# Kernel optimization log

Measured on AMD Instinct MI355X. Metric: run time of the kernel, lower is better.

Reference implementation:

```python
import math
import jax
import jax.numpy as jnp
import numpy as np

N_IMG = 8
A = 3
H = 100
W = 100
STRIDE = 16
IMG = 1600
PRE_NMS_TOP_N = 2000
POST_NMS_TOP_N = 1000
NMS_THRESH = 0.7
MIN_SIZE = 0
BBOX_XFORM_CLIP = math.log(1000.0 / 16.0)


def setup_inputs() -> dict:
    key = jax.random.key(0)
    k1, k2 = jax.random.split(key)
    objectness = jax.random.normal(k1, (N_IMG, A, H, W), jnp.float32)
    box_regression = jax.random.normal(k2, (N_IMG, A * 4, H, W), jnp.float32) * 0.5
    # Grid anchors, flattened in (H, W, A) order to match objectness.permute(0,2,3,1)
    cy = (jnp.arange(H, dtype=jnp.float32) + 0.5) * STRIDE  # [H]
    cx = (jnp.arange(W, dtype=jnp.float32) + 0.5) * STRIDE  # [W]
    half = jnp.array([64.0, 128.0, 256.0], jnp.float32) / 2.0  # [A]
    cy = cy[:, None, None]  # [H,1,1]
    cx = cx[None, :, None]  # [1,W,1]
    s = half[None, None, :]  # [1,1,A]
    x1, y1, x2, y2 = jnp.broadcast_arrays(cx - s, cy - s, cx + s, cy + s)
    anc = jnp.stack([x1, y1, x2, y2], axis=-1).reshape(-1, 4)  # [H*W*A, 4]
    anchors = jnp.broadcast_to(anc[None], (N_IMG, H * W * A, 4)).copy()
    return {
        "objectness": objectness,
        "box_regression": box_regression,
        "anchors": anchors,
        "image_height": IMG,
        "image_width": IMG,
    }


def _decode(deltas, boxes):
    # BoxCoder(weights=(1,1,1,1)).decode with TO_REMOVE=1
    widths = boxes[..., 2] - boxes[..., 0] + 1.0
    heights = boxes[..., 3] - boxes[..., 1] + 1.0
    ctr_x = boxes[..., 0] + 0.5 * widths
    ctr_y = boxes[..., 1] + 0.5 * heights
    dx, dy = deltas[..., 0], deltas[..., 1]
    dw = jnp.minimum(deltas[..., 2], BBOX_XFORM_CLIP)
    dh = jnp.minimum(deltas[..., 3], BBOX_XFORM_CLIP)
    pcx = dx * widths + ctr_x
    pcy = dy * heights + ctr_y
    pw = jnp.exp(dw) * widths
    ph = jnp.exp(dh) * heights
    return jnp.stack(
        [pcx - 0.5 * pw, pcy - 0.5 * ph, pcx + 0.5 * pw - 1.0, pcy + 0.5 * ph - 1.0],
        axis=-1,
    )


def _nms_keep(boxes, valid, thresh):
    # boxes [n,4] sorted by descending score; valid: pre-filter mask.
    n = boxes.shape[0]
    x1, y1, x2, y2 = boxes[:, 0], boxes[:, 1], boxes[:, 2], boxes[:, 3]
    areas = (x2 - x1 + 1.0) * (y2 - y1 + 1.0)
    xx1 = jnp.maximum(x1[:, None], x1[None, :])
    yy1 = jnp.maximum(y1[:, None], y1[None, :])
    xx2 = jnp.minimum(x2[:, None], x2[None, :])
    yy2 = jnp.minimum(y2[:, None], y2[None, :])
    inter = jnp.maximum(xx2 - xx1 + 1.0, 0.0) * jnp.maximum(yy2 - yy1 + 1.0, 0.0)
    iou = inter / (areas[:, None] + areas[None, :] - inter)
    idx = jnp.arange(n)

    def body(i, keep):
        sup = keep[i] & (iou[i] > thresh) & (idx > i)
        return keep & ~sup

    return jax.lax.fori_loop(0, n, body, valid)


def _forward(objectness, box_regression, anchors, image_height, image_width):
    N, A_, H_, W_ = objectness.shape
    scores = jax.nn.sigmoid(objectness.transpose(0, 2, 3, 1).reshape(N, -1))  # [N, A*H*W]
    deltas = (
        box_regression.reshape(N, A_, 4, H_, W_)
        .transpose(0, 3, 4, 1, 2)
        .reshape(N, -1, 4)
    )
    pre = min(PRE_NMS_TOP_N, scores.shape[1])
    top_scores, top_idx = jax.lax.top_k(scores, pre)  # sorted descending
    deltas = jnp.take_along_axis(deltas, top_idx[:, :, None], axis=1)
    anc = jnp.take_along_axis(anchors, top_idx[:, :, None], axis=1)
    props = _decode(deltas, anc)  # [N, pre, 4]
    # clip to image (fact = 1)
    xs = jnp.clip(props[..., 0::2], 0.0, image_width - 1.0)
    ys = jnp.clip(props[..., 1::2], 0.0, image_height - 1.0)
    props = jnp.stack([xs[..., 0], ys[..., 0], xs[..., 1], ys[..., 1]], axis=-1)
    # filter small / out-of-image-center boxes
    ws = props[..., 2] - props[..., 0] + 1.0
    hs = props[..., 3] - props[..., 1] + 1.0
    xc = props[..., 0] + ws / 2.0
    yc = props[..., 1] + hs / 2.0
    valid = (ws >= MIN_SIZE) & (hs >= MIN_SIZE) & (xc < image_width) & (yc < image_height)
    keep = jax.vmap(lambda b, v: _nms_keep(b, v, NMS_THRESH))(props, valid)

    def _select(b, s, k):
        # compact kept boxes (already score-sorted) into fixed-size output
        rank = jnp.cumsum(k) - 1
        tgt = jnp.where(k & (rank < POST_NMS_TOP_N), rank, POST_NMS_TOP_N)
        ob = jnp.zeros((POST_NMS_TOP_N + 1, 4), b.dtype).at[tgt].set(b)[:POST_NMS_TOP_N]
        os = jnp.zeros((POST_NMS_TOP_N + 1,), s.dtype).at[tgt].set(s)[:POST_NMS_TOP_N]
        ov = jnp.arange(POST_NMS_TOP_N) < jnp.minimum(jnp.sum(k), POST_NMS_TOP_N)
        return ob, os, ov

    return jax.vmap(_select)(props, top_scores, keep)


def reference(objectness, box_regression, anchors, image_height, image_width):
    # Returns (boxes [N,post,4], objectness scores [N,post], valid mask [N,post])
    return _forward(objectness, box_regression, anchors, image_height, image_width)
```

## Files before the change

kernel.cpp:

```cpp
#include <hip/hip_runtime.h>
#include <math.h>
#include <stdint.h>

#define NIMG   8
#define NA     30000
#define NQ4    7500
#define PRE_N  2000
#define POST_N 1000
#define NMS_TH 0.7f
#define DCLIP  4.135166556742356f
#define IMGF   1600.0f
#define IMGM1  1599.0f
#define CAND_MAX 4096
#define HPITCH 4104
#define BIG_BIN 64
#define PREF_BIN 3064u


__device__ __forceinline__ void decode_store(
    uint64_t key, unsigned int rank, int n, const float* __restrict__ breg,
    float* __restrict__ wsBoxes, float* __restrict__ wsScores,
    int* __restrict__ wsValid)
{
    unsigned int idx = (unsigned int)key;
    unsigned int k   = ~((unsigned int)(key >> 32));
    unsigned int u   = (k & 0x80000000u) ? (k & 0x7fffffffu) : ~k;
    float logit = __uint_as_float(u);
    float score = 1.0f / (1.0f + expf(-logit));

    int a = idx % 3, t = idx / 3, w = t % 100, h = t / 100;
    const float* bp = breg + n*120000 + (a*4)*10000 + t;
    float dx = bp[0], dy = bp[10000], dw = bp[20000], dh = bp[30000];

    float half = (a == 0) ? 32.0f : ((a == 1) ? 64.0f : 128.0f);
    float cx = w * 16.0f + 8.0f, cy = h * 16.0f + 8.0f;
    float x1 = cx - half, y1 = cy - half, x2 = cx + half, y2 = cy + half;
    float wd = x2 - x1 + 1.0f, hg = y2 - y1 + 1.0f;
    float cxr = x1 + 0.5f * wd, cyr = y1 + 0.5f * hg;
    dw = fminf(dw, DCLIP); dh = fminf(dh, DCLIP);
    float pcx = dx * wd + cxr, pcy = dy * hg + cyr;
    float pw = expf(dw) * wd, ph = expf(dh) * hg;
    float px1 = pcx - 0.5f * pw, py1 = pcy - 0.5f * ph;
    float px2 = pcx + 0.5f * pw - 1.0f, py2 = pcy + 0.5f * ph - 1.0f;
    px1 = fminf(fmaxf(px1, 0.0f), IMGM1);
    px2 = fminf(fmaxf(px2, 0.0f), IMGM1);
    py1 = fminf(fmaxf(py1, 0.0f), IMGM1);
    py2 = fminf(fmaxf(py2, 0.0f), IMGM1);
    float wss = px2 - px1 + 1.0f, hss = py2 - py1 + 1.0f;
    float xc = px1 + wss * 0.5f, yc = py1 + hss * 0.5f;
    int valid = (wss >= 0.0f) && (hss >= 0.0f) && (xc < IMGF) && (yc < IMGF);

    ((float4*)wsBoxes)[n * PRE_N + (int)rank] = make_float4(px1, py1, px2, py2);
    wsScores[n * PRE_N + (int)rank] = score;
    wsValid [n * PRE_N + (int)rank] = valid;
}

__device__ __forceinline__ unsigned int keyof(float f) {
    unsigned int u = __float_as_uint(f);
    return (u & 0x80000000u) ? ~u : (u | 0x80000000u);
}

__global__ __launch_bounds__(1024) void topk_decode(
    const float* __restrict__ obj, const float* __restrict__ breg,
    float* __restrict__ wsBoxes, float* __restrict__ wsScores,
    int* __restrict__ wsValid)
{
    const int n    = blockIdx.x;
    const int tid  = threadIdx.x;
    const int lane = tid & 63;
    const int wid  = tid >> 6;
    const int rep  = wid & 3;

    __shared__ unsigned int   histf[4 * HPITCH];
    __shared__ unsigned short sufx[4096];
    __shared__ uint64_t       grp[CAND_MAX];
    __shared__ uint64_t       grp2[CAND_MAX];
    __shared__ unsigned int   wsum[16];
    __shared__ unsigned int   sbstar;
    __shared__ unsigned int   lbbase[16];
    __shared__ unsigned int   lbcnt, lbtot;

    unsigned int*   hist2  = histf;
    unsigned short* sufx2  = (unsigned short*)(histf + HPITCH);
    unsigned char*  bin2lb = (unsigned char*)(histf + 2 * HPITCH);

    for (int b = tid; b < 4 * HPITCH; b += 1024) histf[b] = 0u;
    __syncthreads();

    const float4* obj4 = (const float4*)(obj + n * NA);
    float4 v[8];
    #pragma unroll
    for (int kk = 0; kk < 7; ++kk) v[kk] = obj4[tid + kk * 1024];
    v[7] = make_float4(0.f, 0.f, 0.f, 0.f);
    if (tid < NQ4 - 7 * 1024) v[7] = obj4[tid + 7 * 1024];

    #pragma unroll
    for (int kk = 0; kk < 8; ++kk) {
        if (kk == 7 && tid >= NQ4 - 7 * 1024) continue;
        const float fv[4] = {v[kk].x, v[kk].y, v[kk].z, v[kk].w};
        #pragma unroll
        for (int e = 0; e < 4; ++e) {
            unsigned int b = keyof(fv[e]) >> 20;
            if (b >= PREF_BIN)
                atomicAdd(&histf[rep * HPITCH + b], 1u);
        }
    }
    __syncthreads();

    unsigned int c0, c1, c2, c3;
    {
        const int b0 = tid * 4;
        c0 = histf[b0+0] + histf[HPITCH+b0+0] + histf[2*HPITCH+b0+0] + histf[3*HPITCH+b0+0];
        c1 = histf[b0+1] + histf[HPITCH+b0+1] + histf[2*HPITCH+b0+1] + histf[3*HPITCH+b0+1];
        c2 = histf[b0+2] + histf[HPITCH+b0+2] + histf[2*HPITCH+b0+2] + histf[3*HPITCH+b0+2];
        c3 = histf[b0+3] + histf[HPITCH+b0+3] + histf[2*HPITCH+b0+3] + histf[3*HPITCH+b0+3];
    }
    unsigned int p = c0 + c1 + c2 + c3;
    unsigned int s = p;
    #pragma unroll
    for (int off = 1; off < 64; off <<= 1) {
        unsigned int vv = __shfl_down(s, off);
        if (lane + off < 64) s += vv;
    }
    if (lane == 0) wsum[wid] = s;
    __syncthreads();
    unsigned int ftotal = 0;
    for (int w = 0; w < 16; ++w) ftotal += wsum[w];

    if (ftotal < PRE_N) {
        #pragma unroll
        for (int kk = 0; kk < 8; ++kk) {
            if (kk == 7 && tid >= NQ4 - 7 * 1024) continue;
            const float fv[4] = {v[kk].x, v[kk].y, v[kk].z, v[kk].w};
            #pragma unroll
            for (int e = 0; e < 4; ++e) {
                unsigned int b = keyof(fv[e]) >> 20;
                if (b < PREF_BIN)
                    atomicAdd(&histf[rep * HPITCH + b], 1u);
            }
        }
        __syncthreads();
        {
            const int b0 = tid * 4;
            c0 = histf[b0+0] + histf[HPITCH+b0+0] + histf[2*HPITCH+b0+0] + histf[3*HPITCH+b0+0];
            c1 = histf[b0+1] + histf[HPITCH+b0+1] + histf[2*HPITCH+b0+1] + histf[3*HPITCH+b0+1];
            c2 = histf[b0+2] + histf[HPITCH+b0+2] + histf[2*HPITCH+b0+2] + histf[3*HPITCH+b0+2];
            c3 = histf[b0+3] + histf[HPITCH+b0+3] + histf[2*HPITCH+b0+3] + histf[3*HPITCH+b0+3];
        }
        p = c0 + c1 + c2 + c3;
        s = p;
        #pragma unroll
        for (int off = 1; off < 64; off <<= 1) {
            unsigned int vv = __shfl_down(s, off);
            if (lane + off < 64) s += vv;
        }
        __syncthreads();
        if (lane == 0) wsum[wid] = s;
        __syncthreads();
    }

    unsigned int wafter = 0;
    for (int w = wid + 1; w < 16; ++w) wafter += wsum[w];
    unsigned int after = (s - p) + wafter;
    {
        unsigned int S3 = after + c3;
        unsigned int S2 = S3 + c2;
        unsigned int S1 = S2 + c1;
        unsigned int S0 = S1 + c0;
        if (S3 >= PRE_N && after < PRE_N) { sbstar = tid*4+3; }
        if (S2 >= PRE_N && S3    < PRE_N) { sbstar = tid*4+2; }
        if (S1 >= PRE_N && S2    < PRE_N) { sbstar = tid*4+1; }
        if (S0 >= PRE_N && S1    < PRE_N) { sbstar = tid*4+0; }
        sufx[tid*4+0] = (unsigned short)S1;
        sufx[tid*4+1] = (unsigned short)S2;
        sufx[tid*4+2] = (unsigned short)S3;
        sufx[tid*4+3] = (unsigned short)after;

        const unsigned int st[4] = {S1, S2, S3, after};
        #pragma unroll
        for (int q = 0; q < 4; ++q) {
            const int b = tid*4 + q;
            unsigned int base = st[q];
            #pragma unroll
            for (int r = 0; r < 4; ++r) {
                unsigned int c = histf[r * HPITCH + b];
                histf[r * HPITCH + b] = base;
                base += c;
            }
        }
    }
    __syncthreads();
    const unsigned int bstar = sbstar;

    #pragma unroll
    for (int kk = 0; kk < 8; ++kk) {
        if (kk == 7 && tid >= NQ4 - 7 * 1024) continue;
        const float fv[4] = {v[kk].x, v[kk].y, v[kk].z, v[kk].w};
        #pragma unroll
        for (int e = 0; e < 4; ++e) {
            unsigned int k = keyof(fv[e]);
            unsigned int b = k >> 20;
            if (b < bstar) continue;
            int j = (tid + kk * 1024) * 4 + e;
            int a = j / 10000, t = j - a * 10000;
            uint64_t key = (((uint64_t)(~k)) << 32) | (unsigned int)(t * 3 + a);
            unsigned int slot = atomicAdd(&histf[rep * HPITCH + b], 1u);
            if (slot < CAND_MAX) grp[slot] = key;
        }
    }
    __syncthreads();

    const unsigned int total = min(histf[3 * HPITCH + bstar], (unsigned int)CAND_MAX);

    ((unsigned int*)bin2lb)[tid] = 0xFFFFFFFFu;
    hist2[tid] = 0u; hist2[tid+1024] = 0u; hist2[tid+2048] = 0u; hist2[tid+3072] = 0u;
    if (tid == 0) { lbcnt = 0u; lbtot = 0u; }
    __syncthreads();

    #pragma unroll
    for (int q = 0; q < 4; ++q) {
        const unsigned int b = (unsigned int)(tid*4 + q);
        if (b >= bstar) {
            const unsigned int ge  = min(histf[3*HPITCH + b], (unsigned int)CAND_MAX);
            const unsigned int cnt = ge - (unsigned int)sufx[b];
            if (cnt > (unsigned int)BIG_BIN) {
                unsigned int pos = atomicAdd(&lbcnt, 1u);
                if (pos < 16u) {
                    bin2lb[b] = (unsigned char)pos;
                    lbbase[pos] = atomicAdd(&lbtot, cnt);
                }
            }
        }
    }
    __syncthreads();

    for (unsigned int slot = tid; slot < total; slot += 1024) {
        const unsigned int hi = (unsigned int)(grp[slot] >> 32);
        const unsigned int b  = 4095u - (hi >> 20);
        const unsigned char lb = bin2lb[b];
        if (lb != 0xFFu)
            atomicAdd(&hist2[(unsigned int)lb * 256u + ((hi >> 12) & 0xFFu)], 1u);
    }
    __syncthreads();

    {
        const unsigned int nlb = min(lbcnt, 16u);
        if ((unsigned int)wid < nlb) {
            const int xb = wid * 256 + lane * 4;
            unsigned int e0 = hist2[xb+0], e1 = hist2[xb+1],
                         e2 = hist2[xb+2], e3 = hist2[xb+3];
            unsigned int tsum = e0 + e1 + e2 + e3;
            unsigned int inc = tsum;
            #pragma unroll
            for (int off = 1; off < 64; off <<= 1) {
                unsigned int vv = __shfl_up(inc, off);
                if (lane >= off) inc += vv;
            }
            unsigned int base = lbbase[wid] + (inc - tsum);
            hist2[xb+0] = base;             sufx2[xb+0] = (unsigned short)base;
            base += e0; hist2[xb+1] = base; sufx2[xb+1] = (unsigned short)base;
            base += e1; hist2[xb+2] = base; sufx2[xb+2] = (unsigned short)base;
            base += e2; hist2[xb+3] = base; sufx2[xb+3] = (unsigned short)base;
        }
    }
    __syncthreads();

    for (unsigned int slot = tid; slot < total; slot += 1024) {
        const uint64_t key = grp[slot];
        const unsigned int hi = (unsigned int)(key >> 32);
        const unsigned int b  = 4095u - (hi >> 20);
        const unsigned char lb = bin2lb[b];
        if (lb != 0xFFu) {
            unsigned int d = atomicAdd(&hist2[(unsigned int)lb * 256u + ((hi >> 12) & 0xFFu)], 1u);
            grp2[d] = key;
        }
    }
    __syncthreads();

    for (unsigned int slot = tid; slot < total; slot += 1024) {
        const uint64_t key = grp[slot];
        const unsigned int hi = (unsigned int)(key >> 32);
        const unsigned int b  = 4095u - (hi >> 20);
        const unsigned int gbeg = sufx[b];
        const unsigned int gend = min(histf[3 * HPITCH + b], (unsigned int)CAND_MAX);
        const unsigned char lb  = bin2lb[b];
        unsigned int rank;

        if (lb != 0xFFu) {
            const unsigned int x   = (unsigned int)lb * 256u + ((hi >> 12) & 0xFFu);
            const unsigned int s2  = sufx2[x];
            const unsigned int e2v = hist2[x];
            rank = gbeg + (s2 - lbbase[lb]);
            for (unsigned int g = s2; g < e2v; g += 8u) {
                #pragma unroll
                for (int i = 0; i < 8; ++i) {
                    const unsigned int gi = g + (unsigned int)i;
                    const uint64_t vv = grp2[min(gi, e2v - 1u)];
                    rank += (gi < e2v && vv < key) ? 1u : 0u;
                }
            }
        } else {
            rank = gbeg;
            unsigned int g = gbeg;
            for (; g + 8u <= gend; g += 8u) {
                uint64_t v0 = grp[g+0], v1 = grp[g+1], v2 = grp[g+2], v3 = grp[g+3];
                uint64_t v4 = grp[g+4], v5 = grp[g+5], v6 = grp[g+6], v7 = grp[g+7];
                unsigned int r0 = (v0 < key) ? 1u : 0u;
                r0 += (v1 < key) ? 1u : 0u;
                r0 += (v2 < key) ? 1u : 0u;
                r0 += (v3 < key) ? 1u : 0u;
                r0 += (v4 < key) ? 1u : 0u;
                r0 += (v5 < key) ? 1u : 0u;
                r0 += (v6 < key) ? 1u : 0u;
                r0 += (v7 < key) ? 1u : 0u;
                rank += r0;
            }
            for (; g < gend; ++g)
                rank += (grp[g] < key) ? 1u : 0u;
        }
        if (rank >= PRE_N) continue;
        decode_store(key, rank, n, breg, wsBoxes, wsScores, wsValid);
    }
}

__global__ __launch_bounds__(512) void nms_mask(
    const float* __restrict__ wsBoxes, uint64_t* __restrict__ mask)
{
    const int blk  = blockIdx.x;
    const int n    = blk >> 5;
    const int i_t  = blk & 31;
    const int tid  = threadIdx.x;
    const int lane = tid & 63;
    const int wv   = tid >> 6;

    __shared__ uint64_t tile[64 * 33];

    for (int idx = tid; idx < 64 * 33; idx += 512) tile[idx] = 0ull;
    __syncthreads();

    const int r = i_t * 64 + lane;
    float4 rb = (r < PRE_N) ? ((const float4*)wsBoxes)[n * PRE_N + r]
                            : make_float4(0.f, 0.f, 0.f, 0.f);
    float ra = (rb.z - rb.x + 1.0f) * (rb.w - rb.y + 1.0f);

    for (int j_t = i_t + wv; j_t < 32; j_t += 8) {
        const int j = j_t * 64 + lane;
        float4 cb = (j < PRE_N) ? ((const float4*)wsBoxes)[n * PRE_N + j]
                                : make_float4(3e30f, 3e30f, 3e30f, 3e30f);
        float ca = (cb.z - cb.x + 1.0f) * (cb.w - cb.y + 1.0f);
        const uint64_t jmask = (j_t == 31) ? 0xFFFFull : ~0ull;
        const bool diag = (j_t == i_t);
        uint64_t myword = 0ull;

        #pragma unroll
        for (int c = 0; c < 64; ++c) {
            float rx1 = __int_as_float(__builtin_amdgcn_readlane(__float_as_int(rb.x), c));
            float ry1 = __int_as_float(__builtin_amdgcn_readlane(__float_as_int(rb.y), c));
            float rx2 = __int_as_float(__builtin_amdgcn_readlane(__float_as_int(rb.z), c));
            float ry2 = __int_as_float(__builtin_amdgcn_readlane(__float_as_int(rb.w), c));
            float rar = __int_as_float(__builtin_amdgcn_readlane(__float_as_int(ra), c));
            float xx1 = fmaxf(rx1, cb.x), yy1 = fmaxf(ry1, cb.y);
            float xx2 = fminf(rx2, cb.z), yy2 = fminf(ry2, cb.w);
            float ww = fmaxf(xx2 - xx1 + 1.0f, 0.0f);
            float hh = fmaxf(yy2 - yy1 + 1.0f, 0.0f);
            float inter = ww * hh;
            float denom = rar + ca - inter;
            unsigned long long bits = __ballot(inter > NMS_TH * denom) & jmask;
            if (diag) bits &= (c == 63) ? 0ull : ((~0ull) << (c + 1));
            if (lane == c) myword = bits;
        }
        tile[lane * 33 + j_t] = myword;
    }
    __syncthreads();

    uint64_t* mrow = mask + ((size_t)n * PRE_N + (size_t)i_t * 64) * 32;
    const int cmax = (i_t == 31) ? 16 : 64;
    for (int idx = tid; idx < cmax * 32; idx += 512) {
        const int rr = idx >> 5, w = idx & 31;
        mrow[idx] = tile[rr * 33 + w];
    }
}

#define SL(n,b) \
    "global_load_dword v" #n ", %[voff], %[sbase]\n\t" \
    "v_add_u32 %[voff], 0x100, %[voff]\n\t"

#define SS(n,b) \
    "s_waitcnt vmcnt(63)\n\t" \
    "v_readlane_b32 %[t], v" #n ", %[lw]\n\t" \
    "s_bitcmp1_b32 %[win], " #b "\n\t" \
    "s_cselect_b32 %[m], 0, -1\n\t" \
    "s_sub_i32 %[kept], %[kept], %[m]\n\t" \
    "s_and_b32 %[t], %[t], %[m]\n\t" \
    "s_or_b32 %[win], %[win], %[t]\n\t" \
    "v_and_b32 v" #n ", %[m], v" #n "\n\t" \
    "v_or_b32 %[rem], %[rem], v" #n "\n\t" \
    "global_load_dword v" #n ", %[voff], %[sbase]\n\t" \
    "v_add_u32 %[voff], 0x100, %[voff]\n\t"

#define SN(n,b,w) \
    "s_waitcnt vmcnt(" #w ")\n\t" \
    "v_readlane_b32 %[t], v" #n ", %[lw]\n\t" \
    "s_bitcmp1_b32 %[win], " #b "\n\t" \
    "s_cselect_b32 %[m], 0, -1\n\t" \
    "s_sub_i32 %[kept], %[kept], %[m]\n\t" \
    "s_and_b32 %[t], %[t], %[m]\n\t" \
    "s_or_b32 %[win], %[win], %[t]\n\t" \
    "v_and_b32 v" #n ", %[m], v" #n "\n\t" \
    "v_or_b32 %[rem], %[rem], v" #n "\n\t"

#define SWIN \
    "s_add_u32 %[lw], %[lw], 1\n\t" \
    "v_readlane_b32 %[t], %[rem], %[lw]\n\t" \
    "s_mov_b32 %[win], %[t]\n\t"

#define ROW_A(M) M(64,0) M(65,1) M(66,2) M(67,3) M(68,4) M(69,5) M(70,6) M(71,7) \
    M(72,8) M(73,9) M(74,10) M(75,11) M(76,12) M(77,13) M(78,14) M(79,15) \
    M(80,16) M(81,17) M(82,18) M(83,19) M(84,20) M(85,21) M(86,22) M(87,23) \
    M(88,24) M(89,25) M(90,26) M(91,27) M(92,28) M(93,29) M(94,30) M(95,31)
#define ROW_B(M) M(96,0) M(97,1) M(98,2) M(99,3) M(100,4) M(101,5) M(102,6) M(103,7) \
    M(104,8) M(105,9) M(106,10) M(107,11) M(108,12) M(109,13) M(110,14) M(111,15) \
    M(112,16) M(113,17) M(114,18) M(115,19) M(116,20) M(117,21) M(118,22) M(119,23) \
    M(120,24) M(121,25) M(122,26) M(123,27) M(124,28) M(125,29) M(126,30) M(127,31)

__global__ __launch_bounds__(256) void nms_scan_select(
    const float* __restrict__ wsBoxes, const float* __restrict__ wsScores,
    const int* __restrict__ wsValid, const uint64_t* __restrict__ mask,
    float* __restrict__ out)
{
    const int n   = blockIdx.x;
    const int tid = threadIdx.x;

    __shared__ __align__(8) unsigned char invb[256];
    __shared__ unsigned int keepw32[64];
    __shared__ int sscan[256];

    unsigned int byte = 0xFFu;
    if (tid < PRE_N / 8) {
        byte = 0u;
        for (int q = 0; q < 8; ++q)
            byte |= (wsValid[n * PRE_N + tid * 8 + q] ? 0u : 1u) << q;
    }
    invb[tid] = (unsigned char)byte;
    __syncthreads();

    if (tid < 64) {
        unsigned int rem = ((const unsigned int*)invb)[tid];
        unsigned long long sbase =
            (unsigned long long)(const void*)(mask + (size_t)n * PRE_N * 32);
        unsigned int voff = (unsigned int)(tid * 4);
        int win_, m_, t_, lw_, kept_, cnt_;

        asm volatile(
            "s_waitcnt vmcnt(0) lgkmcnt(0)\n\t"
            "s_mov_b32 %[kept], 0\n\t"
            "s_mov_b32 %[lw], 0\n\t"
            ROW_A(SL) ROW_B(SL)
            "v_readlane_b32 %[t], %[rem], %[lw]\n\t"
            "s_mov_b32 %[win], %[t]\n\t"
            "s_mov_b32 %[cnt], 30\n\t"
            "Lnms_%=:\n\t"
            ROW_A(SS)
            SWIN
            ROW_B(SS)
            SWIN
            "s_cmp_ge_i32 %[kept], 0x3e8\n\t"
            "s_cbranch_scc1 Lend_%=\n\t"
            "s_sub_u32 %[cnt], %[cnt], 1\n\t"
            "s_cmp_lg_u32 %[cnt], 0\n\t"
            "s_cbranch_scc1 Lnms_%=\n\t"
            SS(64,0) SS(65,1) SS(66,2) SS(67,3) SS(68,4) SS(69,5) SS(70,6) SS(71,7)
            SS(72,8) SS(73,9) SS(74,10) SS(75,11) SS(76,12) SS(77,13) SS(78,14) SS(79,15)
            SN(80,16,63) SN(81,17,62) SN(82,18,61) SN(83,19,60)
            SN(84,20,59) SN(85,21,58) SN(86,22,57) SN(87,23,56)
            SN(88,24,55) SN(89,25,54) SN(90,26,53) SN(91,27,52)
            SN(92,28,51) SN(93,29,50) SN(94,30,49) SN(95,31,48)
            SWIN
            SN(96,0,47) SN(97,1,46) SN(98,2,45) SN(99,3,44)
            SN(100,4,43) SN(101,5,42) SN(102,6,41) SN(103,7,40)
            SN(104,8,39) SN(105,9,38) SN(106,10,37) SN(107,11,36)
            SN(108,12,35) SN(109,13,34) SN(110,14,33) SN(111,15,32)
            SN(112,16,31) SN(113,17,30) SN(114,18,29) SN(115,19,28)
            SN(116,20,27) SN(117,21,26) SN(118,22,25) SN(119,23,24)
            SN(120,24,23) SN(121,25,22) SN(122,26,21) SN(123,27,20)
            SN(124,28,19) SN(125,29,18) SN(126,30,17) SN(127,31,16)
            SWIN
            SN(64,0,15) SN(65,1,14) SN(66,2,13) SN(67,3,12)
            SN(68,4,11) SN(69,5,10) SN(70,6,9) SN(71,7,8)
            SN(72,8,7) SN(73,9,6) SN(74,10,5) SN(75,11,4)
            SN(76,12,3) SN(77,13,2) SN(78,14,1) SN(79,15,0)
            "Lend_%=:\n\t"
            "s_waitcnt vmcnt(0)\n\t"
            : [rem]"+v"(rem), [voff]"+v"(voff),
              [win]"=&s"(win_), [m]"=&s"(m_), [t]"=&s"(t_),
              [lw]"=&s"(lw_), [kept]"=&s"(kept_), [cnt]"=&s"(cnt_)
            : [sbase]"s"(sbase)
            : "scc", "vcc", "memory",
              "v64","v65","v66","v67","v68","v69","v70","v71",
              "v72","v73","v74","v75","v76","v77","v78","v79",
              "v80","v81","v82","v83","v84","v85","v86","v87",
              "v88","v89","v90","v91","v92","v93","v94","v95",
              "v96","v97","v98","v99","v100","v101","v102","v103",
              "v104","v105","v106","v107","v108","v109","v110","v111",
              "v112","v113","v114","v115","v116","v117","v118","v119",
              "v120","v121","v122","v123","v124","v125","v126","v127");

        keepw32[tid] = ~rem;
    }
    __syncthreads();

    int c[8]; const int base8 = tid * 8;
    int lsum = 0;
    for (int q = 0; q < 8; ++q) {
        const int i = base8 + q;
        c[q] = (i < PRE_N) ? (int)((keepw32[i >> 5] >> (i & 31)) & 1u) : 0;
        lsum += c[q];
    }
    sscan[tid] = lsum;
    __syncthreads();
    for (int off = 1; off < 256; off <<= 1) {
        int v = (tid >= off) ? sscan[tid - off] : 0;
        __syncthreads();
        sscan[tid] += v;
        __syncthreads();
    }
    const int excl  = sscan[tid] - lsum;
    const int total = sscan[255];

    float* ob  = out + n * POST_N * 4;
    float* osc = out + NIMG * POST_N * 4 + n * POST_N;
    float* ovd = out + NIMG * POST_N * 5 + n * POST_N;

    for (int i = tid; i < POST_N * 4; i += 256) ob[i] = 0.0f;
    for (int i = tid; i < POST_N; i += 256) osc[i] = 0.0f;
    const int lim = min(total, POST_N);
    for (int i = tid; i < POST_N; i += 256) ovd[i] = (i < lim) ? 1.0f : 0.0f;
    __syncthreads();

    int run = excl;
    for (int q = 0; q < 8; ++q) {
        const int i = base8 + q;
        if (i < PRE_N && c[q]) {
            if (run < POST_N) {
                float4 b = ((const float4*)wsBoxes)[n * PRE_N + i];
                ob[run * 4 + 0] = b.x;
                ob[run * 4 + 1] = b.y;
                ob[run * 4 + 2] = b.z;
                ob[run * 4 + 3] = b.w;
                osc[run] = wsScores[n * PRE_N + i];
            }
            run++;
        }
    }
}

extern "C" void kernel_launch(void* const* d_in, const int* in_sizes, int n_in,
                              void* d_out, int out_size, void* d_ws, size_t ws_size,
                              hipStream_t stream) {
    const float* obj  = (const float*)d_in[0];
    const float* breg = (const float*)d_in[1];
    float* ws        = (float*)d_ws;
    float* wsBoxes   = ws;
    float* wsScores  = ws + 64000;
    int*   wsValid   = (int*)(ws + 80000);
    uint64_t* wsMask = (uint64_t*)(ws + 96000);

    topk_decode<<<NIMG, 1024, 0, stream>>>(obj, breg, wsBoxes, wsScores, wsValid);
    nms_mask<<<NIMG * 32, 512, 0, stream>>>(wsBoxes, wsMask);
    nms_scan_select<<<NIMG, 256, 0, stream>>>(wsBoxes, wsScores, wsValid, wsMask,
                                              (float*)d_out);
}
```

Measured before the change: 153.0 us.

## Replace serial asm NMS scan with block-parallel 64-box group propagation

Replaces the single-wave hand-written assembly scan, which streamed every mask word through one wavefront, with a scheme built on 64-box groups. For each group, wave 0 resolves suppression inside the group from the diagonal mask words using readlane. All 512 threads then OR the kept rows' mask words into a shared suppression bitmap for the later groups using atomics. This targets the serial memory-latency chain of the old scan and reads only the rows of kept boxes. In exchange it adds two block barriers per group and shared-memory atomic contention.

```diff
diff --git a/kernel.cpp b/kernel.cpp
--- a/kernel.cpp
+++ b/kernel.cpp
@@ -381,175 +381,148 @@
     }
 }
 
-#define SL(n,b) \
-    "global_load_dword v" #n ", %[voff], %[sbase]\n\t" \
-    "v_add_u32 %[voff], 0x100, %[voff]\n\t"
-
-#define SS(n,b) \
-    "s_waitcnt vmcnt(63)\n\t" \
-    "v_readlane_b32 %[t], v" #n ", %[lw]\n\t" \
-    "s_bitcmp1_b32 %[win], " #b "\n\t" \
-    "s_cselect_b32 %[m], 0, -1\n\t" \
-    "s_sub_i32 %[kept], %[kept], %[m]\n\t" \
-    "s_and_b32 %[t], %[t], %[m]\n\t" \
-    "s_or_b32 %[win], %[win], %[t]\n\t" \
-    "v_and_b32 v" #n ", %[m], v" #n "\n\t" \
-    "v_or_b32 %[rem], %[rem], v" #n "\n\t" \
-    "global_load_dword v" #n ", %[voff], %[sbase]\n\t" \
-    "v_add_u32 %[voff], 0x100, %[voff]\n\t"
-
-#define SN(n,b,w) \
-    "s_waitcnt vmcnt(" #w ")\n\t" \
-    "v_readlane_b32 %[t], v" #n ", %[lw]\n\t" \
-    "s_bitcmp1_b32 %[win], " #b "\n\t" \
-    "s_cselect_b32 %[m], 0, -1\n\t" \
-    "s_sub_i32 %[kept], %[kept], %[m]\n\t" \
-    "s_and_b32 %[t], %[t], %[m]\n\t" \
-    "s_or_b32 %[win], %[win], %[t]\n\t" \
-    "v_and_b32 v" #n ", %[m], v" #n "\n\t" \
-    "v_or_b32 %[rem], %[rem], v" #n "\n\t"
-
-#define SWIN \
-    "s_add_u32 %[lw], %[lw], 1\n\t" \
-    "v_readlane_b32 %[t], %[rem], %[lw]\n\t" \
-    "s_mov_b32 %[win], %[t]\n\t"
-
-#define ROW_A(M) M(64,0) M(65,1) M(66,2) M(67,3) M(68,4) M(69,5) M(70,6) M(71,7) \
-    M(72,8) M(73,9) M(74,10) M(75,11) M(76,12) M(77,13) M(78,14) M(79,15) \
-    M(80,16) M(81,17) M(82,18) M(83,19) M(84,20) M(85,21) M(86,22) M(87,23) \
-    M(88,24) M(89,25) M(90,26) M(91,27) M(92,28) M(93,29) M(94,30) M(95,31)
-#define ROW_B(M) M(96,0) M(97,1) M(98,2) M(99,3) M(100,4) M(101,5) M(102,6) M(103,7) \
-    M(104,8) M(105,9) M(106,10) M(107,11) M(108,12) M(109,13) M(110,14) M(111,15) \
-    M(112,16) M(113,17) M(114,18) M(115,19) M(116,20) M(117,21) M(118,22) M(119,23) \
-    M(120,24) M(121,25) M(122,26) M(123,27) M(124,28) M(125,29) M(126,30) M(127,31)
-
-__global__ __launch_bounds__(256) void nms_scan_select(
+__global__ __launch_bounds__(512) void nms_scan_select(
     const float* __restrict__ wsBoxes, const float* __restrict__ wsScores,
     const int* __restrict__ wsValid, const uint64_t* __restrict__ mask,
     float* __restrict__ out)
 {
-    const int n   = blockIdx.x;
-    const int tid = threadIdx.x;
-
-    __shared__ __align__(8) unsigned char invb[256];
-    __shared__ unsigned int keepw32[64];
+    const int n    = blockIdx.x;
+    const int tid  = threadIdx.x;
+    const int lane = tid & 63;
+    const int wid  = tid >> 6;
+
+    __shared__ unsigned int sup[64];
+    __shared__ unsigned int kml, kmh;
+    __shared__ int skept, sdone;
     __shared__ int sscan[256];
 
-    unsigned int byte = 0xFFu;
-    if (tid < PRE_N / 8) {
-        byte = 0u;
-        for (int q = 0; q < 8; ++q)
-            byte |= (wsValid[n * PRE_N + tid * 8 + q] ? 0u : 1u) << q;
-    }
-    invb[tid] = (unsigned char)byte;
-    __syncthreads();
-
-    if (tid < 64) {
-        unsigned int rem = ((const unsigned int*)invb)[tid];
-        unsigned long long sbase =
-            (unsigned long long)(const void*)(mask + (size_t)n * PRE_N * 32);
-        unsigned int voff = (unsigned int)(tid * 4);
-        int win_, m_, t_, lw_, kept_, cnt_;
-
-        asm volatile(
-            "s_waitcnt vmcnt(0) lgkmcnt(0)\n\t"
-            "s_mov_b32 %[kept], 0\n\t"
-            "s_mov_b32 %[lw], 0\n\t"
-            ROW_A(SL) ROW_B(SL)
-            "v_readlane_b32 %[t], %[rem], %[lw]\n\t"
-            "s_mov_b32 %[win], %[t]\n\t"
-            "s_mov_b32 %[cnt], 30\n\t"
-            "Lnms_%=:\n\t"
-            ROW_A(SS)
-            SWIN
-            ROW_B(SS)
-            SWIN
-            "s_cmp_ge_i32 %[kept], 0x3e8\n\t"
-            "s_cbranch_scc1 Lend_%=\n\t"
-            "s_sub_u32 %[cnt], %[cnt], 1\n\t"
-            "s_cmp_lg_u32 %[cnt], 0\n\t"
-            "s_cbranch_scc1 Lnms_%=\n\t"
-            SS(64,0) SS(65,1) SS(66,2) SS(67,3) SS(68,4) SS(69,5) SS(70,6) SS(71,7)
-            SS(72,8) SS(73,9) SS(74,10) SS(75,11) SS(76,12) SS(77,13) SS(78,14) SS(79,15)
-            SN(80,16,63) SN(81,17,62) SN(82,18,61) SN(83,19,60)
-            SN(84,20,59) SN(85,21,58) SN(86,22,57) SN(87,23,56)
-            SN(88,24,55) SN(89,25,54) SN(90,26,53) SN(91,27,52)
-            SN(92,28,51) SN(93,29,50) SN(94,30,49) SN(95,31,48)
-            SWIN
-            SN(96,0,47) SN(97,1,46) SN(98,2,45) SN(99,3,44)
-            SN(100,4,43) SN(101,5,42) SN(102,6,41) SN(103,7,40)
-            SN(104,8,39) SN(105,9,38) SN(106,10,37) SN(107,11,36)
-            SN(108,12,35) SN(109,13,34) SN(110,14,33) SN(111,15,32)
-            SN(112,16,31) SN(113,17,30) SN(114,18,29) SN(115,19,28)
-            SN(116,20,27) SN(117,21,26) SN(118,22,25) SN(119,23,24)
-            SN(120,24,23) SN(121,25,22) SN(122,26,21) SN(123,27,20)
-            SN(124,28,19) SN(125,29,18) SN(126,30,17) SN(127,31,16)
-            SWIN
-            SN(64,0,15) SN(65,1,14) SN(66,2,13) SN(67,3,12)
-            SN(68,4,11) SN(69,5,10) SN(70,6,9) SN(71,7,8)
-            SN(72,8,7) SN(73,9,6) SN(74,10,5) SN(75,11,4)
-            SN(76,12,3) SN(77,13,2) SN(78,14,1) SN(79,15,0)
-            "Lend_%=:\n\t"
-            "s_waitcnt vmcnt(0)\n\t"
-            : [rem]"+v"(rem), [voff]"+v"(voff),
-              [win]"=&s"(win_), [m]"=&s"(m_), [t]"=&s"(t_),
-              [lw]"=&s"(lw_), [kept]"=&s"(kept_), [cnt]"=&s"(cnt_)
-            : [sbase]"s"(sbase)
-            : "scc", "vcc", "memory",
-              "v64","v65","v66","v67","v68","v69","v70","v71",
-              "v72","v73","v74","v75","v76","v77","v78","v79",
-              "v80","v81","v82","v83","v84","v85","v86","v87",
-              "v88","v89","v90","v91","v92","v93","v94","v95",
-              "v96","v97","v98","v99","v100","v101","v102","v103",
-              "v104","v105","v106","v107","v108","v109","v110","v111",
-              "v112","v113","v114","v115","v116","v117","v118","v119",
-              "v120","v121","v122","v123","v124","v125","v126","v127");
-
-        keepw32[tid] = ~rem;
-    }
-    __syncthreads();
-
-    int c[8]; const int base8 = tid * 8;
+    if (tid < 64) sup[tid] = 0u;
+    if (tid == 0) { skept = 0; sdone = 0; }
+    __syncthreads();
+
+    if (tid < 500) {
+        int4 vv = ((const int4*)(wsValid + n * PRE_N))[tid];
+        unsigned int nib = (vv.x ? 0u : 1u) | ((vv.y ? 0u : 1u) << 1)
+                         | ((vv.z ? 0u : 1u) << 2) | ((vv.w ? 0u : 1u) << 3);
+        if (nib) atomicOr(&sup[tid >> 3], nib << ((tid & 7) * 4));
+    } else {
+        atomicOr(&sup[tid >> 3], 0xFu << ((tid & 7) * 4));
+    }
+    __syncthreads();
+
+    const uint64_t* mrow = mask + (size_t)n * PRE_N * 32;
+
+    unsigned int cl = 0u, ch = 0u;
+    if (wid == 0) {
+        uint64_t cw = (lane < PRE_N) ? mrow[(size_t)lane * 32 + 0] : 0ull;
+        cl = (unsigned int)cw; ch = (unsigned int)(cw >> 32);
+    }
+
+    for (int g = 0; g < 32; ++g) {
+        __syncthreads();
+        if (sdone) break;
+
+        if (wid == 0) {
+            unsigned int nl = 0u, nh = 0u;
+            if (g < 31) {
+                const int r = (g + 1) * 64 + lane;
+                uint64_t cw = (r < PRE_N) ? mrow[(size_t)r * 32 + (g + 1)] : 0ull;
+                nl = (unsigned int)cw; nh = (unsigned int)(cw >> 32);
+            }
+
+            unsigned long long win =
+                ((unsigned long long)sup[2*g + 1] << 32) | sup[2*g];
+            #pragma unroll
+            for (int b = 0; b < 64; ++b) {
+                unsigned long long t =
+                    ((unsigned long long)(unsigned int)__builtin_amdgcn_readlane((int)ch, b) << 32)
+                    | (unsigned int)__builtin_amdgcn_readlane((int)cl, b);
+                unsigned long long dead = (win >> b) & 1ull;
+                win |= t & (dead - 1ull);
+            }
+            unsigned long long km = ~win;
+            if (lane == 0) {
+                sup[2*g]     = (unsigned int)win;
+                sup[2*g + 1] = (unsigned int)(win >> 32);
+                kml = (unsigned int)km;
+                kmh = (unsigned int)(km >> 32);
+                int nk = skept + __popcll(km);
+                skept = nk;
+                if (nk >= POST_N) sdone = 1;
+            }
+            cl = nl; ch = nh;
+        }
+        __syncthreads();
+
+        if (!sdone) {
+            const int w = tid & 31;
+            if (w > g) {
+                const unsigned long long km =
+                    ((unsigned long long)kmh << 32) | kml;
+                const int r0 = (tid >> 5) * 4;
+                unsigned long long acc = 0ull;
+                #pragma unroll
+                for (int q = 0; q < 4; ++q) {
+                    const int rl = r0 + q;
+                    if ((km >> rl) & 1ull)
+                        acc |= mrow[(size_t)(g * 64 + rl) * 32 + w];
+                }
+                if (acc) {
+                    atomicOr(&sup[2*w],     (unsigned int)acc);
+                    atomicOr(&sup[2*w + 1], (unsigned int)(acc >> 32));
+                }
+            }
+        }
+    }
+    __syncthreads();
+
+    int c[8];
     int lsum = 0;
-    for (int q = 0; q < 8; ++q) {
-        const int i = base8 + q;
-        c[q] = (i < PRE_N) ? (int)((keepw32[i >> 5] >> (i & 31)) & 1u) : 0;
-        lsum += c[q];
-    }
-    sscan[tid] = lsum;
+    const int base8 = tid * 8;
+    if (tid < 256) {
+        for (int q = 0; q < 8; ++q) {
+            const int i = base8 + q;
+            c[q] = (i < PRE_N) ? (int)((~sup[i >> 5] >> (i & 31)) & 1u) : 0;
+            lsum += c[q];
+        }
+        sscan[tid] = lsum;
+    }
     __syncthreads();
     for (int off = 1; off < 256; off <<= 1) {
-        int v = (tid >= off) ? sscan[tid - off] : 0;
-        __syncthreads();
-        sscan[tid] += v;
-        __syncthreads();
-    }
-    const int excl  = sscan[tid] - lsum;
+        int v = 0;
+        if (tid < 256 && tid >= off) v = sscan[tid - off];
+        __syncthreads();
+        if (tid < 256) sscan[tid] += v;
+        __syncthreads();
+    }
+    const int excl  = (tid < 256) ? (sscan[tid] - lsum) : 0;
     const int total = sscan[255];
 
     float* ob  = out + n * POST_N * 4;
     float* osc = out + NIMG * POST_N * 4 + n * POST_N;
     float* ovd = out + NIMG * POST_N * 5 + n * POST_N;
 
-    for (int i = tid; i < POST_N * 4; i += 256) ob[i] = 0.0f;
-    for (int i = tid; i < POST_N; i += 256) osc[i] = 0.0f;
+    for (int i = tid; i < POST_N * 4; i += 512) ob[i] = 0.0f;
+    for (int i = tid; i < POST_N; i += 512) osc[i] = 0.0f;
     const int lim = min(total, POST_N);
-    for (int i = tid; i < POST_N; i += 256) ovd[i] = (i < lim) ? 1.0f : 0.0f;
-    __syncthreads();
-
-    int run = excl;
-    for (int q = 0; q < 8; ++q) {
-        const int i = base8 + q;
-        if (i < PRE_N && c[q]) {
-            if (run < POST_N) {
-                float4 b = ((const float4*)wsBoxes)[n * PRE_N + i];
-                ob[run * 4 + 0] = b.x;
-                ob[run * 4 + 1] = b.y;
-                ob[run * 4 + 2] = b.z;
-                ob[run * 4 + 3] = b.w;
-                osc[run] = wsScores[n * PRE_N + i];
-            }
-            run++;
+    for (int i = tid; i < POST_N; i += 512) ovd[i] = (i < lim) ? 1.0f : 0.0f;
+    __syncthreads();
+
+    if (tid < 256) {
+        int run = excl;
+        for (int q = 0; q < 8; ++q) {
+            const int i = base8 + q;
+            if (i < PRE_N && c[q]) {
+                if (run < POST_N) {
+                    float4 b = ((const float4*)wsBoxes)[n * PRE_N + i];
+                    ob[run * 4 + 0] = b.x;
+                    ob[run * 4 + 1] = b.y;
+                    ob[run * 4 + 2] = b.z;
+                    ob[run * 4 + 3] = b.w;
+                    osc[run] = wsScores[n * PRE_N + i];
+                }
+                run++;
+            }
         }
     }
 }
@@ -567,6 +540,6 @@
 
     topk_decode<<<NIMG, 1024, 0, stream>>>(obj, breg, wsBoxes, wsScores, wsValid);
     nms_mask<<<NIMG * 32, 512, 0, stream>>>(wsBoxes, wsMask);
-    nms_scan_select<<<NIMG, 256, 0, stream>>>(wsBoxes, wsScores, wsValid, wsMask,
+    nms_scan_select<<<NIMG, 512, 0, stream>>>(wsBoxes, wsScores, wsValid, wsMask,
                                               (float*)d_out);
 }
```

Measured after the change: 169.5 us. 10.8% more time.
